# Performance work log

Measured on AMD Instinct MI355X. Metric: run time of the kernel, lower is better.

## Reference

```python
import jax, jax.numpy as jnp
import numpy as np

N = 50000          # num nodes
DEG = 16           # fixed degree (uniform CSR)
E = N * DEG        # num edges
R = 8              # num relations
IN = 128
HID = 128
OUT = 40
BN_EPS = 1e-5


def setup_inputs() -> dict:
    key = jax.random.key(0)
    k = jax.random.split(key, 5)
    x = jax.random.normal(k[0], (N, IN), jnp.float32)
    # glorot-ish init for per-relation weights
    W1 = jax.random.normal(k[1], (R, IN, HID), jnp.float32) * (2.0 / (IN + HID)) ** 0.5
    W2 = jax.random.normal(k[2], (R, HID, OUT), jnp.float32) * (2.0 / (HID + OUT)) ** 0.5
    ptr = jnp.arange(N + 1, dtype=jnp.int32) * DEG            # CSR row offsets
    idx = jax.random.randint(k[3], (E,), 0, N, jnp.int32)     # neighbor (src) ids
    edge_types = jax.random.randint(k[4], (E,), 0, R, jnp.int32)
    return {
        "x": x, "W1": W1, "W2": W2,
        "bn_gamma": jnp.ones((HID,), jnp.float32),
        "bn_beta": jnp.zeros((HID,), jnp.float32),
        "bn_mean": jnp.zeros((HID,), jnp.float32),
        "bn_var": jnp.ones((HID,), jnp.float32),
        "ptr": ptr, "idx": idx, "edge_types": edge_types,
    }


def _rgcn_layer(h, W, ptr, idx, edge_types):
    # RGCNOP: out[i] = sum_{e in [ptr[i],ptr[i+1])} x[idx[e]] @ W[etype[e]]
    # Efficient form: transform every node by every relation once, then gather
    # the (src, etype) pair per edge and scatter-add into destinations.
    xr = jnp.einsum('nd,rdh->nrh', h, W)             # [N, R, H]
    msgs = xr[idx, edge_types]                       # [E, H] irregular gather
    deg = ptr[1:] - ptr[:-1]                         # [N]
    dst = jnp.repeat(jnp.arange(ptr.shape[0] - 1, dtype=jnp.int32), deg,
                     total_repeat_length=idx.shape[0])
    agg = jax.ops.segment_sum(msgs, dst, num_segments=ptr.shape[0] - 1)
    return agg / deg[:, None].astype(agg.dtype)      # degree normalization


def reference(x, W1, W2, bn_gamma, bn_beta, bn_mean, bn_var, ptr, idx, edge_types):
    h = _rgcn_layer(x, W1, ptr, idx, edge_types)
    # BatchNorm1d in eval mode (history_size=0, dropout inactive)
    h = (h - bn_mean) * jax.lax.rsqrt(bn_var + BN_EPS) * bn_gamma + bn_beta
    h = jax.nn.relu(h)
    h = _rgcn_layer(h, W2, ptr, idx, edge_types)
    return jax.nn.log_softmax(h, axis=-1)
```

## Files before the change

### kernel.cpp

```cpp
#include <hip/hip_runtime.h>
#include <math.h>

typedef __attribute__((ext_vector_type(8))) short bf16x8;
typedef __attribute__((ext_vector_type(4))) float f32x4;

constexpr int kN   = 50000;
constexpr int kIn  = 128;
constexpr int kHid = 128;
constexpr int kOut = 40;
constexpr int kNT  = 16;
constexpr int kLds = 1032;
constexpr float kBnEps = 1e-5f;

__device__ inline float bf2f(ushort s) { return __uint_as_float(((uint)s) << 16); }

__device__ __forceinline__ ushort f2bf(float x) {
    uint u = __float_as_uint(x);
    u += 0x7FFFu + ((u >> 16) & 1u);
    return (ushort)(u >> 16);
}

__device__ __forceinline__ uint cvtpk(float a, float b) {
    uint r;
    asm("v_cvt_pk_bf16_f32 %0, %1, %2" : "=v"(r) : "v"(a), "v"(b));
    return r;
}

__device__ __forceinline__ void pack_unit(const float* __restrict__ W,
                                          ushort* __restrict__ dst,
                                          int N, int frag, int lane)
{
    const int kt = frag & 31;
    const int nt = frag >> 5;
    const int n  = nt * 16 + (lane & 15);
    const int q  = lane >> 4;
    float f[8];
    #pragma unroll
    for (int j = 0; j < 8; ++j) {
        const int k = kt * 32 + q * 8 + j;
        f[j] = (n < N) ? W[(size_t)k * N + n] : 0.f;
    }
    const size_t o = ((size_t)frag * 64 + lane) * 8;
    *(uint4*)&dst[o] = make_uint4(cvtpk(f[0], f[1]), cvtpk(f[2], f[3]),
                                  cvtpk(f[4], f[5]), cvtpk(f[6], f[7]));
}

__global__ __launch_bounds__(256)
void prep(const float* __restrict__ x,  ushort* __restrict__ xb,
          const float* __restrict__ W1, ushort* __restrict__ W1hi,
          const float* __restrict__ W2, ushort* __restrict__ W2hi)
{
    const int b   = blockIdx.x;
    const int tid = threadIdx.x;
    if (b < 3125) {
        const size_t i = ((size_t)b * 256 + tid) * 8;
        const float4 v0 = *(const float4*)&x[i];
        const float4 v1 = *(const float4*)&x[i + 4];
        *(uint4*)&xb[i] = make_uint4(cvtpk(v0.x, v0.y), cvtpk(v0.z, v0.w),
                                     cvtpk(v1.x, v1.y), cvtpk(v1.z, v1.w));
    } else if (b < 3125 + 64) {
        pack_unit(W1, W1hi, kHid, (b - 3125) * 4 + (tid >> 6), tid & 63);
    } else {
        const int frag = (b - 3189) * 4 + (tid >> 6);
        if (frag < 96) pack_unit(W2, W2hi, kOut, frag, tid & 63);
    }
}


__device__ __forceinline__ void stage_fast(const char* fb, int vi, char* msW,
                                           int hOff, int lane)
{
    const int b = (lane & 7) * 16;
    #pragma unroll
    for (int u = 0; u < 4; ++u) {
        const int e   = u * 8 + (lane >> 3);
        const int src = __shfl(vi, e, 64);
        const uint4 v = *(const uint4*)(fb + (((size_t)(uint)src) << 8) + hOff + b);
        *(uint4*)(msW + e * 128 + (b ^ (u << 5))) = v;
    }
}

__device__ __forceinline__ void stage_slow(const char* fb,
                                           const int* __restrict__ idx,
                                           int p0, int p1, int deg0, int deg1,
                                           char* msW, int hOff, int lane)
{
    const int l31 = lane & 31;
    if (lane < 32) {
        for (int e = 0; e < 32; ++e) {
            const bool eok = (e < 16) ? (e < deg0) : ((e - 16) < deg1);
            uint val = 0;
            if (eok) {
                const int g = (e < 16) ? (p0 + e) : (p1 + (e - 16));
                const int s = idx[g];
                val = *(const uint*)(fb + (((size_t)(uint)s) << 8) + hOff + l31 * 4);
            }
            *(uint*)(msW + e * 128 + ((l31 * 4) ^ (((e >> 3) & 3) << 5))) = val;
        }
    }
}

__device__ __forceinline__ bf16x8 readB(const char* msW, int q, int m, int ntL)
{
    const char* ap = msW + q * 1024 + 2 * m + (((ntL ^ q) & 3) << 5);
    bf16x8 b;
    #pragma unroll
    for (int j = 0; j < 8; ++j) b[j] = *(const short*)(ap + j * 128);
    return b;
}

__device__ __forceinline__ void mfma_store(bf16x8 aS, bf16x8 bb, int fbase,
                                           int ntL, int w, int q, int m,
                                           ushort (*aggHi)[kLds])
{
    f32x4 z = {0.f, 0.f, 0.f, 0.f};
    const f32x4 d = __builtin_amdgcn_mfma_f32_16x16x32_bf16(aS, bb, z, 0, 0, 0);
    ushort* dst = &aggHi[2 * w + (q >> 1)][0];
    const int fcol = fbase + ntL * 16 + m;
    const int rb   = (q & 1) * 4;
    dst[(rb + 0) * 128 + fcol] = f2bf(d[0]);
    dst[(rb + 1) * 128 + fcol] = f2bf(d[1]);
    dst[(rb + 2) * 128 + fcol] = f2bf(d[2]);
    dst[(rb + 3) * 128 + fcol] = f2bf(d[3]);
}

__device__ __forceinline__ void phaseA_mfma(const ushort* __restrict__ feat,
                                            const int* __restrict__ ptr,
                                            const int* __restrict__ idx,
                                            const int* __restrict__ etype,
                                            int base, ushort (*aggHi)[kLds],
                                            char* msgs)
{
    const int lane = threadIdx.x & 63;
    const int w    = threadIdx.x >> 6;
    const int m    = lane & 15;
    const int q    = lane >> 4;
    const char* fb = (const char*)feat;

    const int node0 = base + 2 * w;
    const int p0 = ptr[node0];
    const int p1 = ptr[node0 + 1];
    const int p2 = ptr[node0 + 2];
    const int deg0 = p1 - p0, deg1 = p2 - p1;
    const bool fast = (deg0 == 16) && (deg1 == 16);

    const int vi = idx  [p0 + (lane & 31)];
    const int ve = etype[p0 + (lane & 31)];

    char* msW = msgs + w * 4096;

    int code;
    if (fast) {
        code = (((lane & 31) >> 4) << 3) | ve;
    } else {
        const int l31 = lane & 31;
        const bool eok = (l31 < 16) ? (l31 < deg0) : ((l31 - 16) < deg1);
        code = eok ? (((l31 >> 4) << 3) | ve) : 0xFF;
    }

    bf16x8 aS;
    #pragma unroll
    for (int j = 0; j < 8; ++j) {
        const int cj = __shfl(code, q * 8 + j, 64);
        aS[j] = (cj == m) ? (short)0x3F80 : (short)0;
    }

    if (fast) stage_fast(fb, vi, msW, 0, lane);
    else      stage_slow(fb, idx, p0, p1, deg0, deg1, msW, 0, lane);
    const bf16x8 b0 = readB(msW, q, m, 0);
    const bf16x8 b1 = readB(msW, q, m, 1);
    const bf16x8 b2 = readB(msW, q, m, 2);
    const bf16x8 b3 = readB(msW, q, m, 3);

    if (fast) stage_fast(fb, vi, msW, 128, lane);
    else      stage_slow(fb, idx, p0, p1, deg0, deg1, msW, 128, lane);

    mfma_store(aS, b0, 0, 0, w, q, m, aggHi);
    mfma_store(aS, b1, 0, 1, w, q, m, aggHi);
    mfma_store(aS, b2, 0, 2, w, q, m, aggHi);
    mfma_store(aS, b3, 0, 3, w, q, m, aggHi);

    const bf16x8 c0 = readB(msW, q, m, 0);
    const bf16x8 c1 = readB(msW, q, m, 1);
    const bf16x8 c2 = readB(msW, q, m, 2);
    const bf16x8 c3 = readB(msW, q, m, 3);
    mfma_store(aS, c0, 64, 0, w, q, m, aggHi);
    mfma_store(aS, c1, 64, 1, w, q, m, aggHi);
    mfma_store(aS, c2, 64, 2, w, q, m, aggHi);
    mfma_store(aS, c3, 64, 3, w, q, m, aggHi);
}

__global__ __launch_bounds__(512, 4)
void rgcn_layer1(const ushort* __restrict__ xb,
                 const ushort* __restrict__ W1hi,
                 const float* __restrict__ gamma, const float* __restrict__ beta,
                 const float* __restrict__ mean,  const float* __restrict__ var,
                 const int* __restrict__ ptr, const int* __restrict__ idx,
                 const int* __restrict__ etype,
                 ushort* __restrict__ h1b)
{
    __shared__ ushort aggHi[kNT][kLds];
    __shared__ __align__(16) char msgs[8 * 4096];
    const int tid  = threadIdx.x;
    const int base = blockIdx.x * kNT;

    phaseA_mfma(xb, ptr, idx, etype, base, aggHi, msgs);
    __syncthreads();

    const int lane = tid & 63;
    const int wid  = tid >> 6;
    const int m    = lane & 15;
    const int q    = lane >> 4;

    const bf16x8* Bh = (const bf16x8*)W1hi + (size_t)wid * 32 * 64 + lane;
    f32x4 acc = {0.f, 0.f, 0.f, 0.f};

    #pragma unroll 4
    for (int kt = 0; kt < 32; ++kt) {
        const bf16x8 ah = *(const bf16x8*)&aggHi[m][kt * 32 + q * 8];
        const bf16x8 bh = Bh[(size_t)kt * 64];
        acc = __builtin_amdgcn_mfma_f32_16x16x32_bf16(ah, bh, acc, 0, 0, 0);
    }

    const int c = wid * 16 + m;
    const float g  = gamma[c] * rsqrtf(var[c] + kBnEps);
    const float mu = mean[c];
    const float bt = beta[c];
    float v[4];
    #pragma unroll
    for (int i = 0; i < 4; ++i) {
        const int node = base + q * 4 + i;
        const float invdeg = 1.0f / (float)(ptr[node + 1] - ptr[node]);
        v[i] = fmaxf((acc[i] * invdeg - mu) * g + bt, 0.f);
    }
    const uint p01 = cvtpk(v[0], v[1]);
    const uint p23 = cvtpk(v[2], v[3]);
    const int n0 = base + q * 4;
    h1b[(size_t)(n0 + 0) * kHid + c] = (ushort)(p01 & 0xFFFFu);
    h1b[(size_t)(n0 + 1) * kHid + c] = (ushort)(p01 >> 16);
    h1b[(size_t)(n0 + 2) * kHid + c] = (ushort)(p23 & 0xFFFFu);
    h1b[(size_t)(n0 + 3) * kHid + c] = (ushort)(p23 >> 16);
}

__global__ __launch_bounds__(512, 4)
void rgcn_layer2(const ushort* __restrict__ h1b,
                 const ushort* __restrict__ W2hi,
                 const int* __restrict__ ptr, const int* __restrict__ idx,
                 const int* __restrict__ etype,
                 float* __restrict__ out)
{
    __shared__ ushort aggHi[kNT][kLds];
    __shared__ __align__(16) char msgs[8 * 4096];
    __shared__ float logits[kNT][48];
    const int tid  = threadIdx.x;
    const int base = blockIdx.x * kNT;

    phaseA_mfma(h1b, ptr, idx, etype, base, aggHi, msgs);
    __syncthreads();

    const int lane = tid & 63;
    const int wid  = tid >> 6;
    const int m    = lane & 15;
    const int q    = lane >> 4;

    if (wid < 3) {
        const bf16x8* Bh = (const bf16x8*)W2hi + (size_t)wid * 32 * 64 + lane;
        f32x4 acc = {0.f, 0.f, 0.f, 0.f};
        #pragma unroll 4
        for (int kt = 0; kt < 32; ++kt) {
            const bf16x8 ah = *(const bf16x8*)&aggHi[m][kt * 32 + q * 8];
            const bf16x8 bh = Bh[(size_t)kt * 64];
            acc = __builtin_amdgcn_mfma_f32_16x16x32_bf16(ah, bh, acc, 0, 0, 0);
        }
        const int n = wid * 16 + m;
        if (n < kOut) {
            #pragma unroll
            for (int i = 0; i < 4; ++i) {
                const int node = base + q * 4 + i;
                const float invdeg = 1.0f / (float)(ptr[node + 1] - ptr[node]);
                logits[q * 4 + i][n] = acc[i] * invdeg;
            }
        }
    }
    __syncthreads();

    #pragma unroll
    for (int i = 0; i < 2; ++i) {
        const int nrow = wid * 2 + i;
        const int node = base + nrow;
        const float v = (lane < kOut) ? logits[nrow][lane] : -INFINITY;
        float mx = v;
        #pragma unroll
        for (int off = 32; off > 0; off >>= 1)
            mx = fmaxf(mx, __shfl_xor(mx, off, 64));
        float s = (lane < kOut) ? __expf(v - mx) : 0.f;
        #pragma unroll
        for (int off = 32; off > 0; off >>= 1)
            s += __shfl_xor(s, off, 64);
        if (lane < kOut)
            out[(size_t)node * kOut + lane] = v - mx - __logf(s);
    }
}

extern "C" void kernel_launch(void* const* d_in, const int* in_sizes, int n_in,
                              void* d_out, int out_size, void* d_ws, size_t ws_size,
                              hipStream_t stream)
{
    const float* x     = (const float*)d_in[0];
    const float* W1    = (const float*)d_in[1];
    const float* W2    = (const float*)d_in[2];
    const float* gamma = (const float*)d_in[3];
    const float* beta  = (const float*)d_in[4];
    const float* mean  = (const float*)d_in[5];
    const float* var   = (const float*)d_in[6];
    const int*   ptr   = (const int*)d_in[7];
    const int*   idx   = (const int*)d_in[8];
    const int*   et    = (const int*)d_in[9];
    float*       out   = (float*)d_out;

    char* ws = (char*)d_ws;
    ushort* h1b  = (ushort*)ws;
    ushort* xb   = (ushort*)(ws + 12800000);
    ushort* W1hi = (ushort*)(ws + 25600000);
    ushort* W2hi = (ushort*)(ws + 25600000 + 262144);

    prep<<<dim3(3125 + 64 + 24), dim3(256), 0, stream>>>(x, xb, W1, W1hi, W2, W2hi);

    dim3 grid(kN / kNT), block(512);
    rgcn_layer1<<<grid, block, 0, stream>>>(xb, W1hi, gamma, beta, mean, var,
                                            ptr, idx, et, h1b);
    rgcn_layer2<<<grid, block, 0, stream>>>(h1b, W2hi, ptr, idx, et, out);
}
```

Baseline: 196.6 us.

## Precompute per-relation layer-2 transforms in layer 1, gather transformed rows in layer 2

Result: faster. 184.9 us (-5.9%).

```diff
diff --git a/kernel.cpp b/kernel.cpp
--- a/kernel.cpp
+++ b/kernel.cpp
@@ -12,6 +12,12 @@
 constexpr int kLds = 1032;
 constexpr float kBnEps = 1e-5f;
 
+constexpr size_t kOffW2hi = 262144;
+constexpr size_t kOffW2z  = 360448;
+constexpr size_t kOffXb   = 524288;
+constexpr size_t kOffBig  = 13324288;
+constexpr size_t kZBytes  = (size_t)kN * 512 * 2;
+
 __device__ inline float bf2f(ushort s) { return __uint_as_float(((uint)s) << 16); }
 
 __device__ __forceinline__ ushort f2bf(float x) {
@@ -25,6 +31,8 @@
     asm("v_cvt_pk_bf16_f32 %0, %1, %2" : "=v"(r) : "v"(a), "v"(b));
     return r;
 }
+
+#define RD(V, J) __builtin_amdgcn_readlane((V), (J))
 
 __device__ __forceinline__ void pack_unit(const float* __restrict__ W,
                                           ushort* __restrict__ dst,
@@ -48,7 +56,8 @@
 __global__ __launch_bounds__(256)
 void prep(const float* __restrict__ x,  ushort* __restrict__ xb,
           const float* __restrict__ W1, ushort* __restrict__ W1hi,
-          const float* __restrict__ W2, ushort* __restrict__ W2hi)
+          const float* __restrict__ W2, ushort* __restrict__ W2hi,
+          ushort* __restrict__ W2z, int useZ)
 {
     const int b   = blockIdx.x;
     const int tid = threadIdx.x;
@@ -60,12 +69,29 @@
                                      cvtpk(v1.x, v1.y), cvtpk(v1.z, v1.w));
     } else if (b < 3125 + 64) {
         pack_unit(W1, W1hi, kHid, (b - 3125) * 4 + (tid >> 6), tid & 63);
-    } else {
+    } else if (b < 3213) {
         const int frag = (b - 3189) * 4 + (tid >> 6);
         if (frag < 96) pack_unit(W2, W2hi, kOut, frag, tid & 63);
-    }
-}
-
+    } else if (useZ) {
+        const int frag = (b - 3213) * 4 + (tid >> 6);
+        const int kt   = frag & 3;
+        const int nt   = frag >> 2;
+        const int lane = tid & 63;
+        const int c    = nt * 16 + (lane & 15);
+        const int r    = c >> 6;
+        const int o    = c & 63;
+        const int q    = lane >> 4;
+        float f[8];
+        #pragma unroll
+        for (int j = 0; j < 8; ++j) {
+            const int k = kt * 32 + q * 8 + j;
+            f[j] = (o < kOut) ? W2[((size_t)r * kHid + k) * kOut + o] : 0.f;
+        }
+        const size_t of = ((size_t)frag * 64 + lane) * 8;
+        *(uint4*)&W2z[of] = make_uint4(cvtpk(f[0], f[1]), cvtpk(f[2], f[3]),
+                                       cvtpk(f[4], f[5]), cvtpk(f[6], f[7]));
+    }
+}
 
 __device__ __forceinline__ void stage_fast(const char* fb, int vi, char* msW,
                                            int hOff, int lane)
@@ -193,11 +219,12 @@
 __global__ __launch_bounds__(512, 4)
 void rgcn_layer1(const ushort* __restrict__ xb,
                  const ushort* __restrict__ W1hi,
+                 const ushort* __restrict__ W2z,
                  const float* __restrict__ gamma, const float* __restrict__ beta,
                  const float* __restrict__ mean,  const float* __restrict__ var,
                  const int* __restrict__ ptr, const int* __restrict__ idx,
                  const int* __restrict__ etype,
-                 ushort* __restrict__ h1b)
+                 ushort* __restrict__ big, int useZ)
 {
     __shared__ ushort aggHi[kNT][kLds];
     __shared__ __align__(16) char msgs[8 * 4096];
@@ -235,11 +262,46 @@
     }
     const uint p01 = cvtpk(v[0], v[1]);
     const uint p23 = cvtpk(v[2], v[3]);
-    const int n0 = base + q * 4;
-    h1b[(size_t)(n0 + 0) * kHid + c] = (ushort)(p01 & 0xFFFFu);
-    h1b[(size_t)(n0 + 1) * kHid + c] = (ushort)(p01 >> 16);
-    h1b[(size_t)(n0 + 2) * kHid + c] = (ushort)(p23 & 0xFFFFu);
-    h1b[(size_t)(n0 + 3) * kHid + c] = (ushort)(p23 >> 16);
+
+    if (useZ) {
+        ushort (*h1lds)[136] = (ushort (*)[136])(msgs + 16384);
+        h1lds[q * 4 + 0][c] = (ushort)(p01 & 0xFFFFu);
+        h1lds[q * 4 + 1][c] = (ushort)(p01 >> 16);
+        h1lds[q * 4 + 2][c] = (ushort)(p23 & 0xFFFFu);
+        h1lds[q * 4 + 3][c] = (ushort)(p23 >> 16);
+        __syncthreads();
+
+        ushort (*zlds)[512] = (ushort (*)[512])msgs;
+        const bf16x8* B2 = (const bf16x8*)W2z;
+        #pragma unroll
+        for (int t = 0; t < 4; ++t) {
+            const int nt = wid * 4 + t;
+            f32x4 a2 = {0.f, 0.f, 0.f, 0.f};
+            #pragma unroll
+            for (int kt2 = 0; kt2 < 4; ++kt2) {
+                const bf16x8 ah2 = *(const bf16x8*)&h1lds[m][kt2 * 32 + q * 8];
+                const bf16x8 bh2 = B2[(size_t)(nt * 4 + kt2) * 64 + lane];
+                a2 = __builtin_amdgcn_mfma_f32_16x16x32_bf16(ah2, bh2, a2, 0, 0, 0);
+            }
+            zlds[q * 4 + 0][nt * 16 + m] = f2bf(a2[0]);
+            zlds[q * 4 + 1][nt * 16 + m] = f2bf(a2[1]);
+            zlds[q * 4 + 2][nt * 16 + m] = f2bf(a2[2]);
+            zlds[q * 4 + 3][nt * 16 + m] = f2bf(a2[3]);
+        }
+        __syncthreads();
+
+        const int row = tid >> 5;
+        const int cs  = (tid & 31) * 16;
+        ushort* zp = big + ((size_t)(base + row)) * 512 + cs;
+        *(uint4*)zp       = *(const uint4*)&zlds[row][cs];
+        *(uint4*)(zp + 8) = *(const uint4*)&zlds[row][cs + 8];
+    } else {
+        const int n0 = base + q * 4;
+        big[(size_t)(n0 + 0) * kHid + c] = (ushort)(p01 & 0xFFFFu);
+        big[(size_t)(n0 + 1) * kHid + c] = (ushort)(p01 >> 16);
+        big[(size_t)(n0 + 2) * kHid + c] = (ushort)(p23 & 0xFFFFu);
+        big[(size_t)(n0 + 3) * kHid + c] = (ushort)(p23 >> 16);
+    }
 }
 
 __global__ __launch_bounds__(512, 4)
@@ -299,6 +361,63 @@
             s += __shfl_xor(s, off, 64);
         if (lane < kOut)
             out[(size_t)node * kOut + lane] = v - mx - __logf(s);
+    }
+}
+
+__global__ __launch_bounds__(256)
+void rgcn_layer2z(const ushort* __restrict__ z,
+                  const int* __restrict__ ptr, const int* __restrict__ idx,
+                  const int* __restrict__ etype,
+                  float* __restrict__ out)
+{
+    const int lane = threadIdx.x & 63;
+    const int wv   = threadIdx.x >> 6;
+    const int n0   = blockIdx.x * 16 + wv * 4;
+
+    const int p0 = ptr[n0];
+    const int d0 = ptr[n0 + 1] - p0;
+    const int d1 = ptr[n0 + 2] - ptr[n0 + 1];
+    const int d2 = ptr[n0 + 3] - ptr[n0 + 2];
+    const int d3 = ptr[n0 + 4] - ptr[n0 + 3];
+    const bool fast = (d0 == 16) & (d1 == 16) & (d2 == 16) & (d3 == 16);
+
+    int vi = 0, ve = 0;
+    if (fast) { vi = idx[p0 + lane]; ve = etype[p0 + lane]; }
+
+    #pragma unroll
+    for (int t = 0; t < 4; ++t) {
+        const int node = n0 + t;
+        float acc = 0.f;
+        float invdeg;
+        if (fast) {
+            invdeg = 0.0625f;
+            #pragma unroll
+            for (int j = 0; j < 16; ++j) {
+                const int e = t * 16 + j;
+                const int s = RD(vi, e);
+                const int r = RD(ve, e);
+                acc += bf2f(z[(size_t)(uint)s * 512 + r * 64 + lane]);
+            }
+        } else {
+            const int pa = ptr[node], pb = ptr[node + 1];
+            invdeg = 1.0f / (float)(pb - pa);
+            for (int e = pa; e < pb; ++e) {
+                const int s = __builtin_amdgcn_readfirstlane(idx[e]);
+                const int r = __builtin_amdgcn_readfirstlane(etype[e]);
+                acc += bf2f(z[(size_t)(uint)s * 512 + r * 64 + lane]);
+            }
+        }
+        const float v = (lane < kOut) ? acc * invdeg : -INFINITY;
+        float mx = v;
+        #pragma unroll
+        for (int off = 32; off > 0; off >>= 1)
+            mx = fmaxf(mx, __shfl_xor(mx, off, 64));
+        float s2 = (lane < kOut) ? __expf(v - mx) : 0.f;
+        #pragma unroll
+        for (int off = 32; off > 0; off >>= 1)
+            s2 += __shfl_xor(s2, off, 64);
+        if (lane < kOut)
+            out[(size_t)node * kOut + lane] = v - mx - __logf(s2);
     }
 }
 
@@ -319,15 +438,24 @@
     float*       out   = (float*)d_out;
 
     char* ws = (char*)d_ws;
-    ushort* h1b  = (ushort*)ws;
-    ushort* xb   = (ushort*)(ws + 12800000);
-    ushort* W1hi = (ushort*)(ws + 25600000);
-    ushort* W2hi = (ushort*)(ws + 25600000 + 262144);
-
-    prep<<<dim3(3125 + 64 + 24), dim3(256), 0, stream>>>(x, xb, W1, W1hi, W2, W2hi);
+    ushort* W1hi = (ushort*)ws;
+    ushort* W2hi = (ushort*)(ws + kOffW2hi);
+    ushort* W2z  = (ushort*)(ws + kOffW2z);
+    ushort* xb   = (ushort*)(ws + kOffXb);
+    ushort* big  = (ushort*)(ws + kOffBig);
+
+    const int useZ = (ws_size >= kOffBig + kZBytes) ? 1 : 0;
+
+    prep<<<dim3(3245), dim3(256), 0, stream>>>(x, xb, W1, W1hi, W2, W2hi,
+                                               W2z, useZ);
 
     dim3 grid(kN / kNT), block(512);
-    rgcn_layer1<<<grid, block, 0, stream>>>(xb, W1hi, gamma, beta, mean, var,
-                                            ptr, idx, et, h1b);
-    rgcn_layer2<<<grid, block, 0, stream>>>(h1b, W2hi, ptr, idx, et, out);
-}
+    rgcn_layer1<<<grid, block, 0, stream>>>(xb, W1hi, W2z, gamma, beta, mean,
+                                            var, ptr, idx, et, big, useZ);
+    if (useZ) {
+        rgcn_layer2z<<<dim3(kN / 16), dim3(256), 0, stream>>>(big, ptr, idx,
+                                                              et, out);
+    } else {
+        rgcn_layer2<<<grid, block, 0, stream>>>(big, W2hi, ptr, idx, et, out);
+    }
+}
```
